# Optimization experiments

Measured on AMD Instinct MI355X. Metric: run time of the kernel, lower is better.

The kernel has to match this reference:

```python
import jax, jax.numpy as jnp
import numpy as np

FEATURE_DIM = 6272
UNITS = 32
B, L = 8, 256

def setup_inputs() -> dict:
    key = jax.random.key(0)
    k1, k2, k3, k4, k5 = jax.random.split(key, 5)
    return {
        "inputs": jax.random.normal(k1, (B, L, FEATURE_DIM), dtype=jnp.float32),
        "Wt": jax.random.normal(k2, (FEATURE_DIM, UNITS), dtype=jnp.float32) * 0.02,
        "bh": jax.random.normal(k3, (UNITS,), dtype=jnp.float32),
        "Wa": jax.random.normal(k4, (UNITS, 1), dtype=jnp.float32) * 0.02,
        "ba": jax.random.normal(k5, (1,), dtype=jnp.float32),
    }

def reference(inputs, Wt, bh, Wa, ba):
    # q == k: both projected through Wt (original code reuses Wt for both)
    p = jnp.einsum('blf,fu->blu', inputs, Wt)            # [B, L, U]
    # additive (Bahdanau-style) pairwise combine: [B, L, L, U]
    beta = jnp.tanh(p[:, :, None, :] + p[:, None, :, :] + bh)
    alpha = jnp.einsum('bqku,uo->bqk', beta, Wa) + ba[0]  # [B, L, L]
    alpha = jax.nn.sigmoid(alpha)
    a = jax.nn.softmax(alpha, axis=-1)                    # softmax over keys
    c_r = jnp.einsum('bqk,bkf->bqf', a, inputs)           # [B, L, F]
    return c_r
```

## Files before the change

kernel.cpp:

```cpp
#include <hip/hip_runtime.h>
#include <hip/hip_bf16.h>
#include <math.h>

#define FDIM 6272
#define LQ   256
#define BN   8
#define UDIM 32
#define BL   (BN*LQ)

typedef short  short8 __attribute__((ext_vector_type(8)));
typedef float  f32x4  __attribute__((ext_vector_type(4)));

static __device__ __forceinline__ ushort f2bf(float f) {
    __hip_bfloat16 h = __float2bfloat16(f);
    return *(ushort*)&h;
}

__global__ __launch_bounds__(256)
void k0_transpose(const float* __restrict__ x, ushort* __restrict__ xt) {
    __shared__ unsigned int xt_s[64 * 33];
    const int t  = threadIdx.x;
    const int f0 = blockIdx.x * 64, k0 = blockIdx.y * 64, b = blockIdx.z;

    const int f4 = t & 15, kr = t >> 4;
    const float* xb = x + ((size_t)b * LQ + k0) * FDIM + f0;

    #pragma unroll
    for (int i = 0; i < 2; ++i) {
        const int kp = kr + 16 * i;
        const float4 v0 = *(const float4*)(xb + (size_t)(2 * kp    ) * FDIM + 4 * f4);
        const float4 v1 = *(const float4*)(xb + (size_t)(2 * kp + 1) * FDIM + 4 * f4);
        xt_s[(4 * f4 + 0) * 33 + kp] = (unsigned)f2bf(v0.x) | ((unsigned)f2bf(v1.x) << 16);
        xt_s[(4 * f4 + 1) * 33 + kp] = (unsigned)f2bf(v0.y) | ((unsigned)f2bf(v1.y) << 16);
        xt_s[(4 * f4 + 2) * 33 + kp] = (unsigned)f2bf(v0.z) | ((unsigned)f2bf(v1.z) << 16);
        xt_s[(4 * f4 + 3) * 33 + kp] = (unsigned)f2bf(v0.w) | ((unsigned)f2bf(v1.w) << 16);
    }
    __syncthreads();

    const int kc8 = t & 7;
    #pragma unroll
    for (int p = 0; p < 2; ++p) {
        const int fr = (t >> 3) + 32 * p;
        uint4 pkt;
        pkt.x = xt_s[fr * 33 + kc8 * 4 + 0];
        pkt.y = xt_s[fr * 33 + kc8 * 4 + 1];
        pkt.z = xt_s[fr * 33 + kc8 * 4 + 2];
        pkt.w = xt_s[fr * 33 + kc8 * 4 + 3];
        *(uint4*)(xt + ((size_t)b * FDIM + f0 + fr) * LQ + k0 + kc8 * 8) = pkt;
    }
}

__global__ __launch_bounds__(256)
void k_wtt(const float* __restrict__ Wt, ushort* __restrict__ wtt) {
    const int gid = blockIdx.x * 256 + threadIdx.x;
    const int u = gid / 784, fg = gid % 784;
    ushort v[8];
    #pragma unroll
    for (int j = 0; j < 8; ++j)
        v[j] = f2bf(Wt[(size_t)(8 * fg + j) * UDIM + u]);
    *(uint4*)(wtt + (size_t)u * FDIM + 8 * fg) = *(uint4*)v;
}

__global__ __launch_bounds__(256)
void k1_mfma(const float* __restrict__ x, const ushort* __restrict__ wtt,
             float* __restrict__ pb) {
    __shared__ ushort As[32 * 40];
    __shared__ ushort Bs[32 * 40];

    const int t    = threadIdx.x;
    const int row0 = blockIdx.x * 32;
    const int f0   = blockIdx.y * 896;
    const int wv   = t >> 6, lane = t & 63;
    const int n16  = lane & 15, quad = lane >> 4;
    const int m0   = 16 * (wv & 1), n0 = 16 * (wv >> 1);

    const int srow = t >> 3, sg = t & 7;

    f32x4 acc = (f32x4){0.f, 0.f, 0.f, 0.f};

    for (int c = 0; c < 28; ++c) {
        const int kk = f0 + c * 32;
        __syncthreads();
        const float4 xv = *(const float4*)(x + (size_t)(row0 + srow) * FDIM + kk + 4 * sg);
        uint2 pk;
        pk.x = (unsigned)f2bf(xv.x) | ((unsigned)f2bf(xv.y) << 16);
        pk.y = (unsigned)f2bf(xv.z) | ((unsigned)f2bf(xv.w) << 16);
        *(uint2*)(As + srow * 40 + 4 * sg) = pk;
        *(uint2*)(Bs + srow * 40 + 4 * sg) =
            *(const uint2*)(wtt + (size_t)srow * FDIM + kk + 4 * sg);
        __syncthreads();

        const short8 af = *(const short8*)(As + (m0 + n16) * 40 + quad * 8);
        const short8 bf = *(const short8*)(Bs + (n0 + n16) * 40 + quad * 8);
        acc = __builtin_amdgcn_mfma_f32_16x16x32_bf16(af, bf, acc, 0, 0, 0);
    }

    #pragma unroll
    for (int r = 0; r < 4; ++r)
        atomicAdd(&pb[(size_t)(row0 + m0 + quad * 4 + r) * UDIM + n0 + n16], acc[r]);
}

__global__ __launch_bounds__(256)
void k2_attn(const float* __restrict__ pb, const float* __restrict__ bh,
             const float* __restrict__ Wa, const float* __restrict__ ba,
             ushort* __restrict__ ab) {
    const int bq = blockIdx.x;
    const int b  = bq >> 8;
    const int k  = threadIdx.x;

    __shared__ float pq_s[UDIM];
    __shared__ float wa_s[UDIM];
    __shared__ float pk_s[LQ * 33];
    __shared__ float red[4];

    if (k < UDIM) {
        pq_s[k] = pb[bq * UDIM + k] + bh[k];
        wa_s[k] = Wa[k];
    }
    const float* pbb = pb + (size_t)b * LQ * UDIM;
    #pragma unroll
    for (int i = 0; i < 32; ++i) {
        int idx = k + i * 256;
        pk_s[(idx >> 5) * 33 + (idx & 31)] = pbb[idx];
    }
    __syncthreads();

    const float* pk = &pk_s[k * 33];
    float s = 0.f;
    #pragma unroll
    for (int u = 0; u < UDIM; ++u)
        s = fmaf(tanhf(pq_s[u] + pk[u]), wa_s[u], s);

    const float alpha = 1.f / (1.f + expf(-(s + ba[0])));
    const float e = expf(alpha);

    float v = e;
    #pragma unroll
    for (int m = 1; m < 64; m <<= 1) v += __shfl_xor(v, m, 64);
    if ((k & 63) == 0) red[k >> 6] = v;
    __syncthreads();
    const float tot = red[0] + red[1] + red[2] + red[3];

    ab[(size_t)bq * LQ + k] = f2bf(e / tot);
}

__global__ __launch_bounds__(256)
void k3_mfma(const ushort* __restrict__ xt, const ushort* __restrict__ ab,
             float* __restrict__ out) {
    __shared__ ushort xs[128 * 72];
    __shared__ ushort as_[64 * 72];

    const int t    = threadIdx.x;
    const int f0   = blockIdx.x * 128, q0 = blockIdx.y * 64, b = blockIdx.z;
    const int wv   = t >> 6;
    const int lane = t & 63;
    const int n    = lane & 15;
    const int quad = lane >> 4;

    const ushort* xtb = xt + ((size_t)b * FDIM + f0) * LQ;
    const ushort* abb = ab + ((size_t)b * LQ + q0) * LQ;

    f32x4 acc[8];
    #pragma unroll
    for (int ff = 0; ff < 8; ++ff) acc[ff] = (f32x4){0.f, 0.f, 0.f, 0.f};

    for (int c = 0; c < 4; ++c) {
        const int kk = c * 64;
        __syncthreads();
        #pragma unroll
        for (int j = 0; j < 4; ++j) {
            const int g = t + 256 * j;
            const int r = g >> 3, c8 = g & 7;
            const uint4 v = *(const uint4*)(xtb + (size_t)r * LQ + kk + c8 * 8);
            *(uint4*)(xs + r * 72 + c8 * 8) = v;
        }
        #pragma unroll
        for (int j = 0; j < 2; ++j) {
            const int g = t + 256 * j;
            const int r = g >> 3, c8 = g & 7;
            const uint4 v = *(const uint4*)(abb + (size_t)r * LQ + kk + c8 * 8);
            *(uint4*)(as_ + r * 72 + c8 * 8) = v;
        }
        __syncthreads();

        #pragma unroll
        for (int ks = 0; ks < 64; ks += 32) {
            const short8 af = *(const short8*)(as_ + (16 * wv + n) * 72 + ks + quad * 8);
            #pragma unroll
            for (int ff = 0; ff < 8; ++ff) {
                const short8 bfr = *(const short8*)(xs + (16 * ff + n) * 72 + ks + quad * 8);
                acc[ff] = __builtin_amdgcn_mfma_f32_16x16x32_bf16(af, bfr, acc[ff], 0, 0, 0);
            }
        }
    }

    float* ob = out + ((size_t)b * LQ + q0 + 16 * wv + quad * 4) * FDIM + f0 + n;
    #pragma unroll
    for (int ff = 0; ff < 8; ++ff)
        #pragma unroll
        for (int r = 0; r < 4; ++r)
            ob[(size_t)r * FDIM + 16 * ff] = acc[ff][r];
}

extern "C" void kernel_launch(void* const* d_in, const int* in_sizes, int n_in,
                              void* d_out, int out_size, void* d_ws, size_t ws_size,
                              hipStream_t stream) {
    const float* x  = (const float*)d_in[0];
    const float* Wt = (const float*)d_in[1];
    const float* bh = (const float*)d_in[2];
    const float* Wa = (const float*)d_in[3];
    const float* ba = (const float*)d_in[4];
    float* out = (float*)d_out;

    float*  pb  = (float*)d_ws;
    ushort* ab  = (ushort*)((char*)d_ws + 262144);
    ushort* wtt = (ushort*)((char*)d_ws + 262144 + 1048576);
    ushort* xt  = (ushort*)((char*)d_ws + 262144 + 1048576 + 524288);

    hipMemsetAsync(pb, 0, (size_t)BL * UDIM * sizeof(float), stream);

    k0_transpose<<<dim3(98, 4, 8), 256, 0, stream>>>(x, xt);
    k_wtt<<<98, 256, 0, stream>>>(Wt, wtt);
    k1_mfma<<<dim3(64, 7), 256, 0, stream>>>(x, wtt, pb);
    k2_attn<<<BL, 256, 0, stream>>>(pb, bh, Wa, ba, ab);
    k3_mfma<<<dim3(49, 4, 8), 256, 0, stream>>>(xt, ab, out);
}
```

Before: 165.9 us.

## Fuse input transpose and bf16 conversion into the attention-output GEMM

Drops the separate transpose kernel that wrote a bf16 transposed copy of the inputs. The final GEMM now reads fp32 inputs directly, converts and transposes them into shared memory, and computes a full 256-query by 64-feature tile per block. Attention weights are loaded straight from global memory rather than staged through shared memory. The memset of the projection accumulator is folded into the weight-transpose kernel. This removes a full write and re-read of a transposed input copy and two launches. In exchange there are fewer blocks (784), more accumulators per thread, and strided fp32 loads in the GEMM.

```diff
diff --git a/kernel.cpp b/kernel.cpp
--- a/kernel.cpp
+++ b/kernel.cpp
@@ -17,41 +17,8 @@
 }
 
 __global__ __launch_bounds__(256)
-void k0_transpose(const float* __restrict__ x, ushort* __restrict__ xt) {
-    __shared__ unsigned int xt_s[64 * 33];
-    const int t  = threadIdx.x;
-    const int f0 = blockIdx.x * 64, k0 = blockIdx.y * 64, b = blockIdx.z;
-
-    const int f4 = t & 15, kr = t >> 4;
-    const float* xb = x + ((size_t)b * LQ + k0) * FDIM + f0;
-
-    #pragma unroll
-    for (int i = 0; i < 2; ++i) {
-        const int kp = kr + 16 * i;
-        const float4 v0 = *(const float4*)(xb + (size_t)(2 * kp    ) * FDIM + 4 * f4);
-        const float4 v1 = *(const float4*)(xb + (size_t)(2 * kp + 1) * FDIM + 4 * f4);
-        xt_s[(4 * f4 + 0) * 33 + kp] = (unsigned)f2bf(v0.x) | ((unsigned)f2bf(v1.x) << 16);
-        xt_s[(4 * f4 + 1) * 33 + kp] = (unsigned)f2bf(v0.y) | ((unsigned)f2bf(v1.y) << 16);
-        xt_s[(4 * f4 + 2) * 33 + kp] = (unsigned)f2bf(v0.z) | ((unsigned)f2bf(v1.z) << 16);
-        xt_s[(4 * f4 + 3) * 33 + kp] = (unsigned)f2bf(v0.w) | ((unsigned)f2bf(v1.w) << 16);
-    }
-    __syncthreads();
-
-    const int kc8 = t & 7;
-    #pragma unroll
-    for (int p = 0; p < 2; ++p) {
-        const int fr = (t >> 3) + 32 * p;
-        uint4 pkt;
-        pkt.x = xt_s[fr * 33 + kc8 * 4 + 0];
-        pkt.y = xt_s[fr * 33 + kc8 * 4 + 1];
-        pkt.z = xt_s[fr * 33 + kc8 * 4 + 2];
-        pkt.w = xt_s[fr * 33 + kc8 * 4 + 3];
-        *(uint4*)(xt + ((size_t)b * FDIM + f0 + fr) * LQ + k0 + kc8 * 8) = pkt;
-    }
-}
-
-__global__ __launch_bounds__(256)
-void k_wtt(const float* __restrict__ Wt, ushort* __restrict__ wtt) {
+void k_wtt(const float* __restrict__ Wt, ushort* __restrict__ wtt,
+           float* __restrict__ pb) {
     const int gid = blockIdx.x * 256 + threadIdx.x;
     const int u = gid / 784, fg = gid % 784;
     ushort v[8];
@@ -59,6 +26,9 @@
     for (int j = 0; j < 8; ++j)
         v[j] = f2bf(Wt[(size_t)(8 * fg + j) * UDIM + u]);
     *(uint4*)(wtt + (size_t)u * FDIM + 8 * fg) = *(uint4*)v;
+
+    if (gid < BL * UDIM / 4)
+        ((float4*)pb)[gid] = make_float4(0.f, 0.f, 0.f, 0.f);
 }
 
 __global__ __launch_bounds__(256)
@@ -144,62 +114,68 @@
     ab[(size_t)bq * LQ + k] = f2bf(e / tot);
 }
 
-__global__ __launch_bounds__(256)
-void k3_mfma(const ushort* __restrict__ xt, const ushort* __restrict__ ab,
-             float* __restrict__ out) {
-    __shared__ ushort xs[128 * 72];
-    __shared__ ushort as_[64 * 72];
+__global__ __launch_bounds__(256, 3)
+void k3_fused(const float* __restrict__ x, const ushort* __restrict__ ab,
+              float* __restrict__ out) {
+    __shared__ ushort Bs[64 * 40];
 
     const int t    = threadIdx.x;
-    const int f0   = blockIdx.x * 128, q0 = blockIdx.y * 64, b = blockIdx.z;
+    const int f0   = blockIdx.x * 64;
+    const int b    = blockIdx.y;
     const int wv   = t >> 6;
     const int lane = t & 63;
-    const int n    = lane & 15;
+    const int n16  = lane & 15;
     const int quad = lane >> 4;
 
-    const ushort* xtb = xt + ((size_t)b * FDIM + f0) * LQ;
-    const ushort* abb = ab + ((size_t)b * LQ + q0) * LQ;
+    const int g  = t >> 4;
+    const int kp = t & 15;
 
-    f32x4 acc[8];
+    const float*  xb  = x  + (size_t)b * LQ * FDIM + f0 + 4 * g;
+    const ushort* abb = ab + (size_t)b * LQ * LQ;
+
+    f32x4 acc[4][4];
     #pragma unroll
-    for (int ff = 0; ff < 8; ++ff) acc[ff] = (f32x4){0.f, 0.f, 0.f, 0.f};
+    for (int mf = 0; mf < 4; ++mf)
+        #pragma unroll
+        for (int nf = 0; nf < 4; ++nf)
+            acc[mf][nf] = (f32x4){0.f, 0.f, 0.f, 0.f};
 
-    for (int c = 0; c < 4; ++c) {
-        const int kk = c * 64;
+    for (int c = 0; c < 8; ++c) {
+        const int kc = c * 32;
         __syncthreads();
-        #pragma unroll
-        for (int j = 0; j < 4; ++j) {
-            const int g = t + 256 * j;
-            const int r = g >> 3, c8 = g & 7;
-            const uint4 v = *(const uint4*)(xtb + (size_t)r * LQ + kk + c8 * 8);
-            *(uint4*)(xs + r * 72 + c8 * 8) = v;
-        }
-        #pragma unroll
-        for (int j = 0; j < 2; ++j) {
-            const int g = t + 256 * j;
-            const int r = g >> 3, c8 = g & 7;
-            const uint4 v = *(const uint4*)(abb + (size_t)r * LQ + kk + c8 * 8);
-            *(uint4*)(as_ + r * 72 + c8 * 8) = v;
+        {
+            const float4 v0 = *(const float4*)(xb + (size_t)(kc + 2 * kp    ) * FDIM);
+            const float4 v1 = *(const float4*)(xb + (size_t)(kc + 2 * kp + 1) * FDIM);
+            unsigned* bw = (unsigned*)Bs;
+            bw[(4 * g + 0) * 20 + kp] = (unsigned)f2bf(v0.x) | ((unsigned)f2bf(v1.x) << 16);
+            bw[(4 * g + 1) * 20 + kp] = (unsigned)f2bf(v0.y) | ((unsigned)f2bf(v1.y) << 16);
+            bw[(4 * g + 2) * 20 + kp] = (unsigned)f2bf(v0.z) | ((unsigned)f2bf(v1.z) << 16);
+            bw[(4 * g + 3) * 20 + kp] = (unsigned)f2bf(v0.w) | ((unsigned)f2bf(v1.w) << 16);
         }
         __syncthreads();
 
+        short8 af[4];
         #pragma unroll
-        for (int ks = 0; ks < 64; ks += 32) {
-            const short8 af = *(const short8*)(as_ + (16 * wv + n) * 72 + ks + quad * 8);
+        for (int mf = 0; mf < 4; ++mf)
+            af[mf] = *(const short8*)(abb + (size_t)(64 * wv + 16 * mf + n16) * LQ
+                                      + kc + quad * 8);
+        #pragma unroll
+        for (int nf = 0; nf < 4; ++nf) {
+            const short8 bf = *(const short8*)(Bs + (16 * nf + n16) * 40 + quad * 8);
             #pragma unroll
-            for (int ff = 0; ff < 8; ++ff) {
-                const short8 bfr = *(const short8*)(xs + (16 * ff + n) * 72 + ks + quad * 8);
-                acc[ff] = __builtin_amdgcn_mfma_f32_16x16x32_bf16(af, bfr, acc[ff], 0, 0, 0);
-            }
+            for (int mf = 0; mf < 4; ++mf)
+                acc[mf][nf] = __builtin_amdgcn_mfma_f32_16x16x32_bf16(af[mf], bf, acc[mf][nf], 0, 0, 0);
         }
     }
 
-    float* ob = out + ((size_t)b * LQ + q0 + 16 * wv + quad * 4) * FDIM + f0 + n;
+    float* ob = out + ((size_t)b * LQ + 64 * wv + quad * 4) * FDIM + f0 + n16;
     #pragma unroll
-    for (int ff = 0; ff < 8; ++ff)
+    for (int mf = 0; mf < 4; ++mf)
         #pragma unroll
-        for (int r = 0; r < 4; ++r)
-            ob[(size_t)r * FDIM + 16 * ff] = acc[ff][r];
+        for (int nf = 0; nf < 4; ++nf)
+            #pragma unroll
+            for (int r = 0; r < 4; ++r)
+                ob[(size_t)(16 * mf + r) * FDIM + 16 * nf] = acc[mf][nf][r];
 }
 
 extern "C" void kernel_launch(void* const* d_in, const int* in_sizes, int n_in,
@@ -215,13 +191,9 @@
     float*  pb  = (float*)d_ws;
     ushort* ab  = (ushort*)((char*)d_ws + 262144);
     ushort* wtt = (ushort*)((char*)d_ws + 262144 + 1048576);
-    ushort* xt  = (ushort*)((char*)d_ws + 262144 + 1048576 + 524288);
 
-    hipMemsetAsync(pb, 0, (size_t)BL * UDIM * sizeof(float), stream);
-
-    k0_transpose<<<dim3(98, 4, 8), 256, 0, stream>>>(x, xt);
-    k_wtt<<<98, 256, 0, stream>>>(Wt, wtt);
+    k_wtt<<<98, 256, 0, stream>>>(Wt, wtt, pb);
     k1_mfma<<<dim3(64, 7), 256, 0, stream>>>(x, wtt, pb);
     k2_attn<<<BL, 256, 0, stream>>>(pb, bh, Wa, ba, ab);
-    k3_mfma<<<dim3(49, 4, 8), 256, 0, stream>>>(xt, ab, out);
+    k3_fused<<<dim3(98, 8), 256, 0, stream>>>(x, ab, out);
 }
```

Result: no change. 168.5 us (+1.6%).
